# Kernel tuning notes

Hardware: AMD Instinct MI355X
Metric: run time of the kernel (lower is better)

## Reference

```python
import jax, jax.numpy as jnp
import numpy as np
import math

N_HEADS = 32
N_KV_HEADS = 4
HEAD_DIM = 128
N_REP = N_HEADS // N_KV_HEADS
ROPE_THETA = 10000.0
YARN_SCALE = 80.0
YARN_ALPHA = 1.0
YARN_BETA = 32.0
MAX_SEQ = int(2048 * YARN_SCALE)  # max_seq_len * yarn_scale, as in __init__


def _rope_yarn_cos_sin(S, dim):
    """Numpy (static) version of precompute_rope_yarn, sliced to S positions."""
    inv_freq = 1.0 / ROPE_THETA ** (np.arange(0, dim, 2, dtype=np.float32) / dim)
    wavelengths = 2.0 * math.pi / inv_freq
    r = MAX_SEQ / wavelengths
    gamma = np.clip((r - YARN_ALPHA) / (YARN_BETA - YARN_ALPHA), 0.0, 1.0)
    inv_freq = inv_freq * ((1.0 - gamma) / YARN_SCALE + gamma)
    t = np.arange(S, dtype=np.float32)
    freqs = np.outer(t, inv_freq)                      # [S, dim/2]
    emb = np.concatenate([freqs, freqs], axis=-1)      # [S, dim]
    emb = emb / math.sqrt(0.1 * math.log(YARN_SCALE) + 1.0)
    # broadcast shape [1, S, 1, dim] to apply per-position across heads
    return (jnp.asarray(np.cos(emb))[None, :, None, :],
            jnp.asarray(np.sin(emb))[None, :, None, :])


def _rotate_half(x):
    x1, x2 = jnp.split(x, 2, axis=-1)
    return jnp.concatenate([-x2, x1], axis=-1)


def setup_inputs() -> dict:
    key = jax.random.key(0)
    ks = jax.random.split(key, 5)
    B, S, D = 1, 2048, 4096
    sd = 1.0 / math.sqrt(D)
    return {
        "x": jax.random.normal(ks[0], (B, S, D), dtype=jnp.float32),
        "wq": jax.random.normal(ks[1], (D, N_HEADS * HEAD_DIM), dtype=jnp.float32) * sd,
        "wk": jax.random.normal(ks[2], (D, N_KV_HEADS * HEAD_DIM), dtype=jnp.float32) * sd,
        "wv": jax.random.normal(ks[3], (D, N_KV_HEADS * HEAD_DIM), dtype=jnp.float32) * sd,
        "wo": jax.random.normal(ks[4], (N_HEADS * HEAD_DIM, D), dtype=jnp.float32) * sd,
    }


def reference(x, wq, wk, wv, wo):
    B, S, D = x.shape
    scale = HEAD_DIM ** -0.5
    q = (x @ wq).reshape(B, S, N_HEADS, HEAD_DIM)
    k = (x @ wk).reshape(B, S, N_KV_HEADS, HEAD_DIM)
    v = (x @ wv).reshape(B, S, N_KV_HEADS, HEAD_DIM)
    cos, sin = _rope_yarn_cos_sin(S, HEAD_DIM)         # [1,S,1,Dh]
    q = q * cos + _rotate_half(q) * sin
    k = k * cos + _rotate_half(k) * sin
    # GQA: repeat kv heads to match query heads (repeat_interleave on head dim)
    k = jnp.repeat(k, N_REP, axis=2)
    v = jnp.repeat(v, N_REP, axis=2)
    # [B,H,S,Dh]
    q = q.transpose(0, 2, 1, 3)
    k = k.transpose(0, 2, 1, 3)
    v = v.transpose(0, 2, 1, 3)
    scores = jnp.einsum("bhsd,bhtd->bhst", q, k) * scale
    causal = jnp.tril(jnp.ones((S, S), dtype=bool))
    scores = jnp.where(causal[None, None], scores, jnp.finfo(scores.dtype).min)
    probs = jax.nn.softmax(scores, axis=-1)
    out = jnp.einsum("bhst,bhtd->bhsd", probs, v)
    out = out.transpose(0, 2, 1, 3).reshape(B, S, N_HEADS * HEAD_DIM)
    return out @ wo
```

## Files before the change

kernel.cpp:

```cpp
#include <hip/hip_runtime.h>
#include <math.h>

#define S_LEN 2048
#define D_MODEL 4096
#define NH 32
#define NKV 4
#define HD 128
#define KV_W (NKV * HD)
#define QK_W (D_MODEL + KV_W)
#define QKV_W (QK_W + KV_W)

typedef float f32x4 __attribute__((ext_vector_type(4)));
typedef __bf16 bf16x8 __attribute__((ext_vector_type(8)));

__device__ __forceinline__ void async16(const __bf16* g, __bf16* l) {
    __builtin_amdgcn_global_load_lds(
        (const __attribute__((address_space(1))) unsigned int*)g,
        (__attribute__((address_space(3))) unsigned int*)l, 16, 0, 0);
}

__global__ void cast_f32_bf16(const float* __restrict__ in, __bf16* __restrict__ out, int n) {
    int i = (blockIdx.x * blockDim.x + threadIdx.x) * 4;
    if (i >= n) return;
    float4 v = *reinterpret_cast<const float4*>(in + i);
    out[i + 0] = (__bf16)v.x;
    out[i + 1] = (__bf16)v.y;
    out[i + 2] = (__bf16)v.z;
    out[i + 3] = (__bf16)v.w;
}

__global__ void transpose_cast(const float* __restrict__ in, __bf16* __restrict__ out, int R, int C) {
    __shared__ float tile[32][33];
    int bx = blockIdx.x * 32, by = blockIdx.y * 32;
    int tx = threadIdx.x, ty = threadIdx.y;
#pragma unroll
    for (int i = 0; i < 32; i += 8)
        tile[ty + i][tx] = in[(size_t)(by + ty + i) * C + bx + tx];
    __syncthreads();
#pragma unroll
    for (int i = 0; i < 32; i += 8)
        out[(size_t)(bx + ty + i) * R + by + tx] = (__bf16)tile[tx][ty + i];
}

template <int MODE>
__global__ __launch_bounds__(256, 2) void gemm_bf16(const __bf16* __restrict__ A,
                                                    const __bf16* __restrict__ Bt,
                                                    void* __restrict__ Cp, void* __restrict__ Cp2,
                                                    int M, int N, int K) {
    __shared__ __bf16 a_lds[128 * 32];
    __shared__ __bf16 b_lds[128 * 32];

    const int tid = threadIdx.x;
    const int wave = tid >> 6, lane = tid & 63;
    const int quad = lane >> 4, l16 = lane & 15;
    const int wm = wave & 1, wn = wave >> 1;
    const int m0 = blockIdx.y * 128, n0 = blockIdx.x * 128;

    f32x4 acc[4][4];
#pragma unroll
    for (int i = 0; i < 4; i++)
#pragma unroll
        for (int j = 0; j < 4; j++) acc[i][j] = (f32x4)0.0f;

    const int crow = tid >> 2, ccol = (tid & 3) * 8;
    const __bf16* Ap0 = A + (size_t)(m0 + crow) * K + ccol;
    const __bf16* Ap1 = A + (size_t)(m0 + 64 + crow) * K + ccol;
    const __bf16* Bp0 = Bt + (size_t)(n0 + crow) * K + ccol;
    const __bf16* Bp1 = Bt + (size_t)(n0 + 64 + crow) * K + ccol;

    for (int k0 = 0; k0 < K; k0 += 32) {
        __syncthreads();
        async16(Ap0 + k0, a_lds + tid * 8);
        async16(Ap1 + k0, a_lds + (tid + 256) * 8);
        async16(Bp0 + k0, b_lds + tid * 8);
        async16(Bp1 + k0, b_lds + (tid + 256) * 8);
        __syncthreads();

        bf16x8 afr[4], bfr[4];
#pragma unroll
        for (int i = 0; i < 4; i++)
            afr[i] = *(const bf16x8*)(a_lds + (wm * 64 + i * 16 + l16) * 32 + quad * 8);
#pragma unroll
        for (int j = 0; j < 4; j++)
            bfr[j] = *(const bf16x8*)(b_lds + (wn * 64 + j * 16 + l16) * 32 + quad * 8);
#pragma unroll
        for (int i = 0; i < 4; i++)
#pragma unroll
            for (int j = 0; j < 4; j++)
                acc[i][j] = __builtin_amdgcn_mfma_f32_16x16x32_bf16(afr[i], bfr[j], acc[i][j], 0, 0, 0);
    }

    const bool vregion = (MODE == 1) && (n0 >= QK_W);
#pragma unroll
    for (int i = 0; i < 4; i++)
#pragma unroll
        for (int j = 0; j < 4; j++)
#pragma unroll
            for (int r = 0; r < 4; r++) {
                int gm = m0 + wm * 64 + i * 16 + quad * 4 + r;
                int gn = n0 + wn * 64 + j * 16 + l16;
                float v = acc[i][j][r];
                if constexpr (MODE == 0) {
                    ((float*)Cp)[(size_t)gm * N + gn] = v;
                } else {
                    if (vregion)
                        ((__bf16*)Cp2)[(size_t)(gn - QK_W) * M + gm] = (__bf16)v;
                    else
                        ((__bf16*)Cp)[(size_t)gm * QK_W + gn] = (__bf16)v;
                }
            }
}

__global__ void rope_cast(const __bf16* __restrict__ src, int sPitch, int sOff,
                          __bf16* __restrict__ dst, int dPitch, int H, int total) {
    int idx = blockIdx.x * blockDim.x + threadIdx.x;
    if (idx >= total) return;
    int d = idx & 63;
    int t = idx >> 6;
    int h = t % H;
    int s = t / H;

    float inv = __powf(10000.0f, -(float)d * (1.0f / 64.0f));
    float wl = 6.2831853071795864f / inv;
    float r = 163840.0f / wl;
    float gamma = fminf(fmaxf((r - 1.0f) * (1.0f / 31.0f), 0.0f), 1.0f);
    float adj = inv * ((1.0f - gamma) * (1.0f / 80.0f) + gamma);
    float ang = ((float)s * adj) / 1.1992508365439246f;
    float c = cosf(ang), sn = sinf(ang);

    const __bf16* b = src + (size_t)s * sPitch + sOff + h * HD;
    __bf16* o = dst + (size_t)s * dPitch + h * HD;
    float x1 = (float)b[d], x2 = (float)b[d + 64];
    o[d] = (__bf16)(x1 * c - x2 * sn);
    o[d + 64] = (__bf16)(x2 * c + x1 * sn);
}

__global__ __launch_bounds__(256, 2) void flash_attn(const __bf16* __restrict__ Q,
                                                     const __bf16* __restrict__ Kb,
                                                     const __bf16* __restrict__ Vt,
                                                     __bf16* __restrict__ O) {
    __shared__ __bf16 k_lds[64 * 128];
    __shared__ __bf16 vt_lds[128 * 64];
    __shared__ __bf16 p_lds[128 * 72];

    const int tid = threadIdx.x;
    const int wave = tid >> 6, lane = tid & 63;
    const int quad = lane >> 4, l16 = lane & 15;
    const int h = blockIdx.x;
    const int ty = blockIdx.y;
    const int t = (ty < 8) ? ty : 23 - ty;
    const int qb0 = t * 128;
    const int wrow = wave * 32;
    const int kvh = h >> 3;
    const float sl2e = 0.12752039149672056f;

    bf16x8 qfr[2][4];
#pragma unroll
    for (int mi = 0; mi < 2; mi++)
#pragma unroll
        for (int kk = 0; kk < 4; kk++)
            qfr[mi][kk] = *(const bf16x8*)(Q + (size_t)(qb0 + wrow + mi * 16 + l16) * D_MODEL
                                           + h * HD + kk * 32 + quad * 8);

    f32x4 acc[2][8];
#pragma unroll
    for (int mi = 0; mi < 2; mi++)
#pragma unroll
        for (int dt = 0; dt < 8; dt++) acc[mi][dt] = (f32x4)0.0f;
    float rs[2][4] = {{0.f, 0.f, 0.f, 0.f}, {0.f, 0.f, 0.f, 0.f}};

    const int nk = 2 * t + 2;
    for (int kt = 0; kt < nk; kt++) {
        const int k0 = kt * 64;
        __syncthreads();
#pragma unroll
        for (int it = 0; it < 4; it++) {
            int c = tid + it * 256;
            int krow = c >> 4, kcb = c & 15;
            async16(Kb + (size_t)(k0 + krow) * KV_W + kvh * HD + ((kcb ^ (krow & 15)) << 3),
                    k_lds + c * 8);
            int vrow = c >> 3, vcb = c & 7;
            async16(Vt + (size_t)(kvh * HD + vrow) * S_LEN + k0 + ((vcb ^ (vrow & 7)) << 3),
                    vt_lds + c * 8);
        }
        __syncthreads();

        f32x4 sc[2][4];
#pragma unroll
        for (int mi = 0; mi < 2; mi++)
#pragma unroll
            for (int j = 0; j < 4; j++) sc[mi][j] = (f32x4)0.0f;
#pragma unroll
        for (int j = 0; j < 4; j++)
#pragma unroll
            for (int kk = 0; kk < 4; kk++) {
                bf16x8 kf = *(const bf16x8*)(k_lds + (((j * 16 + l16) << 4) + ((kk * 4 + quad) ^ l16)) * 8);
                sc[0][j] = __builtin_amdgcn_mfma_f32_16x16x32_bf16(qfr[0][kk], kf, sc[0][j], 0, 0, 0);
                sc[1][j] = __builtin_amdgcn_mfma_f32_16x16x32_bf16(qfr[1][kk], kf, sc[1][j], 0, 0, 0);
            }

        const bool hasmask = (kt >= 2 * t);
#pragma unroll
        for (int mi = 0; mi < 2; mi++) {
            int rowb = qb0 + wrow + mi * 16 + quad * 4;
#pragma unroll
            for (int j = 0; j < 4; j++) {
                int kg = k0 + j * 16 + l16;
#pragma unroll
                for (int r = 0; r < 4; r++) {
                    float p = __builtin_amdgcn_exp2f(sc[mi][j][r] * sl2e);
                    if (hasmask && kg > rowb + r) p = 0.0f;
                    rs[mi][r] += p;
                    p_lds[(wrow + mi * 16 + quad * 4 + r) * 72 + j * 16 + l16] = (__bf16)p;
                }
            }
        }

        bf16x8 pf[2][2];
#pragma unroll
        for (int mi = 0; mi < 2; mi++)
#pragma unroll
            for (int kk = 0; kk < 2; kk++)
                pf[mi][kk] = *(const bf16x8*)(p_lds + (wrow + mi * 16 + l16) * 72 + kk * 32 + quad * 8);
#pragma unroll
        for (int dt = 0; dt < 8; dt++)
#pragma unroll
            for (int kk = 0; kk < 2; kk++) {
                bf16x8 vf = *(const bf16x8*)(vt_lds + (((dt * 16 + l16) << 3) + ((kk * 4 + quad) ^ (l16 & 7))) * 8);
                acc[0][dt] = __builtin_amdgcn_mfma_f32_16x16x32_bf16(pf[0][kk], vf, acc[0][dt], 0, 0, 0);
                acc[1][dt] = __builtin_amdgcn_mfma_f32_16x16x32_bf16(pf[1][kk], vf, acc[1][dt], 0, 0, 0);
            }
    }

    float inv_l[2][4];
#pragma unroll
    for (int mi = 0; mi < 2; mi++)
#pragma unroll
        for (int r = 0; r < 4; r++) {
            float s = rs[mi][r];
#pragma unroll
            for (int m = 1; m <= 8; m <<= 1) s += __shfl_xor(s, m, 64);
            inv_l[mi][r] = 1.0f / s;
        }

#pragma unroll
    for (int mi = 0; mi < 2; mi++)
#pragma unroll
        for (int dt = 0; dt < 8; dt++)
#pragma unroll
            for (int r = 0; r < 4; r++) {
                int row = qb0 + wrow + mi * 16 + quad * 4 + r;
                int col = h * HD + dt * 16 + l16;
                O[(size_t)row * D_MODEL + col] = (__bf16)(acc[mi][dt][r] * inv_l[mi][r]);
            }
}

extern "C" void kernel_launch(void* const* d_in, const int* in_sizes, int n_in,
                              void* d_out, int out_size, void* d_ws, size_t ws_size,
                              hipStream_t stream) {
    const float* x = (const float*)d_in[0];
    const float* wq = (const float*)d_in[1];
    const float* wk = (const float*)d_in[2];
    const float* wv = (const float*)d_in[3];
    const float* wo = (const float*)d_in[4];
    float* out = (float*)d_out;

    char* ws = (char*)d_ws;
    size_t off = 0;
    auto alloc = [&](size_t bytes) {
        void* p = ws + off;
        off += (bytes + 255) & ~(size_t)255;
        return p;
    };
    __bf16* xb    = (__bf16*)alloc((size_t)S_LEN * D_MODEL * 2);
    __bf16* wqkvT = (__bf16*)alloc((size_t)QKV_W * D_MODEL * 2);
    __bf16* woT   = (__bf16*)alloc((size_t)D_MODEL * D_MODEL * 2);
    __bf16* qkb   = (__bf16*)alloc((size_t)S_LEN * QK_W * 2);
    __bf16* vtb   = (__bf16*)alloc((size_t)KV_W * S_LEN * 2);
    __bf16* qb    = (__bf16*)alloc((size_t)S_LEN * D_MODEL * 2);
    __bf16* kb    = (__bf16*)alloc((size_t)S_LEN * KV_W * 2);
    __bf16* ob    = (__bf16*)alloc((size_t)S_LEN * D_MODEL * 2);

    cast_f32_bf16<<<(S_LEN * D_MODEL) / (256 * 4), 256, 0, stream>>>(x, xb, S_LEN * D_MODEL);
    transpose_cast<<<dim3(D_MODEL / 32, D_MODEL / 32), dim3(32, 8), 0, stream>>>(wq, wqkvT, D_MODEL, D_MODEL);
    transpose_cast<<<dim3(KV_W / 32, D_MODEL / 32), dim3(32, 8), 0, stream>>>(wk, wqkvT + (size_t)D_MODEL * D_MODEL, D_MODEL, KV_W);
    transpose_cast<<<dim3(KV_W / 32, D_MODEL / 32), dim3(32, 8), 0, stream>>>(wv, wqkvT + (size_t)QK_W * D_MODEL, D_MODEL, KV_W);
    transpose_cast<<<dim3(D_MODEL / 32, D_MODEL / 32), dim3(32, 8), 0, stream>>>(wo, woT, D_MODEL, D_MODEL);

    gemm_bf16<1><<<dim3(QKV_W / 128, S_LEN / 128), 256, 0, stream>>>(xb, wqkvT, qkb, vtb, S_LEN, QKV_W, D_MODEL);

    rope_cast<<<(S_LEN * NH * 64) / 256, 256, 0, stream>>>(qkb, QK_W, 0, qb, D_MODEL, NH, S_LEN * NH * 64);
    rope_cast<<<(S_LEN * NKV * 64) / 256, 256, 0, stream>>>(qkb, QK_W, D_MODEL, kb, KV_W, NKV, S_LEN * NKV * 64);

    flash_attn<<<dim3(NH, 16), 256, 0, stream>>>(qb, kb, vtb, ob);

    gemm_bf16<0><<<dim3(D_MODEL / 128, S_LEN / 128), 256, 0, stream>>>(ob, woT, out, nullptr, S_LEN, D_MODEL, D_MODEL);
}
```

Baseline: 499.2 us.

## Double-buffer GEMM and attention K tiles, vectorize weight transpose

The GEMM now keeps two LDS stages and issues the next K-slice's async loads before computing on the current one, which removes one barrier per iteration. Flash attention double-buffers the K tile: the V load overlaps the QK^T compute and the next K load overlaps the PV compute. The weight transpose kernel moves to 64x64 tiles with float4 loads and bf16x8 stores. The cost is more LDS per block, which could limit occupancy, plus extra barriers in the attention loop.

```diff
diff --git a/kernel.cpp b/kernel.cpp
--- a/kernel.cpp
+++ b/kernel.cpp
@@ -30,16 +30,27 @@
 }
 
 __global__ void transpose_cast(const float* __restrict__ in, __bf16* __restrict__ out, int R, int C) {
-    __shared__ float tile[32][33];
-    int bx = blockIdx.x * 32, by = blockIdx.y * 32;
-    int tx = threadIdx.x, ty = threadIdx.y;
-#pragma unroll
-    for (int i = 0; i < 32; i += 8)
-        tile[ty + i][tx] = in[(size_t)(by + ty + i) * C + bx + tx];
+    __shared__ float tile[64][65];
+    const int tid = threadIdx.x;
+    const int bx = blockIdx.x * 64, by = blockIdx.y * 64;
+#pragma unroll
+    for (int i = 0; i < 4; i++) {
+        int idx = tid + i * 256;
+        int r = idx >> 4, c4 = (idx & 15) * 4;
+        float4 v = *(const float4*)(in + (size_t)(by + r) * C + bx + c4);
+        tile[r][c4 + 0] = v.x; tile[r][c4 + 1] = v.y;
+        tile[r][c4 + 2] = v.z; tile[r][c4 + 3] = v.w;
+    }
     __syncthreads();
 #pragma unroll
-    for (int i = 0; i < 32; i += 8)
-        out[(size_t)(bx + ty + i) * R + by + tx] = (__bf16)tile[tx][ty + i];
+    for (int i = 0; i < 2; i++) {
+        int idx = tid + i * 256;
+        int oc = idx >> 3, r8 = (idx & 7) * 8;
+        bf16x8 v;
+#pragma unroll
+        for (int e = 0; e < 8; e++) v[e] = (__bf16)tile[r8 + e][oc];
+        *(bf16x8*)(out + (size_t)(bx + oc) * R + by + r8) = v;
+    }
 }
 
 template <int MODE>
@@ -47,8 +58,8 @@
                                                     const __bf16* __restrict__ Bt,
                                                     void* __restrict__ Cp, void* __restrict__ Cp2,
                                                     int M, int N, int K) {
-    __shared__ __bf16 a_lds[128 * 32];
-    __shared__ __bf16 b_lds[128 * 32];
+    __shared__ __bf16 a_lds[2][128 * 32];
+    __shared__ __bf16 b_lds[2][128 * 32];
 
     const int tid = threadIdx.x;
     const int wave = tid >> 6, lane = tid & 63;
@@ -68,21 +79,28 @@
     const __bf16* Bp0 = Bt + (size_t)(n0 + crow) * K + ccol;
     const __bf16* Bp1 = Bt + (size_t)(n0 + 64 + crow) * K + ccol;
 
+    async16(Ap0, a_lds[0] + tid * 8);
+    async16(Ap1, a_lds[0] + (tid + 256) * 8);
+    async16(Bp0, b_lds[0] + tid * 8);
+    async16(Bp1, b_lds[0] + (tid + 256) * 8);
+
     for (int k0 = 0; k0 < K; k0 += 32) {
+        const int cur = (k0 >> 5) & 1;
         __syncthreads();
-        async16(Ap0 + k0, a_lds + tid * 8);
-        async16(Ap1 + k0, a_lds + (tid + 256) * 8);
-        async16(Bp0 + k0, b_lds + tid * 8);
-        async16(Bp1 + k0, b_lds + (tid + 256) * 8);
-        __syncthreads();
+        if (k0 + 32 < K) {
+            async16(Ap0 + k0 + 32, a_lds[cur ^ 1] + tid * 8);
+            async16(Ap1 + k0 + 32, a_lds[cur ^ 1] + (tid + 256) * 8);
+            async16(Bp0 + k0 + 32, b_lds[cur ^ 1] + tid * 8);
+            async16(Bp1 + k0 + 32, b_lds[cur ^ 1] + (tid + 256) * 8);
+        }
 
         bf16x8 afr[4], bfr[4];
 #pragma unroll
         for (int i = 0; i < 4; i++)
-            afr[i] = *(const bf16x8*)(a_lds + (wm * 64 + i * 16 + l16) * 32 + quad * 8);
+            afr[i] = *(const bf16x8*)(a_lds[cur] + (wm * 64 + i * 16 + l16) * 32 + quad * 8);
 #pragma unroll
         for (int j = 0; j < 4; j++)
-            bfr[j] = *(const bf16x8*)(b_lds + (wn * 64 + j * 16 + l16) * 32 + quad * 8);
+            bfr[j] = *(const bf16x8*)(b_lds[cur] + (wn * 64 + j * 16 + l16) * 32 + quad * 8);
 #pragma unroll
         for (int i = 0; i < 4; i++)
 #pragma unroll
@@ -139,7 +157,7 @@
                                                      const __bf16* __restrict__ Kb,
                                                      const __bf16* __restrict__ Vt,
                                                      __bf16* __restrict__ O) {
-    __shared__ __bf16 k_lds[64 * 128];
+    __shared__ __bf16 k_lds[2][64 * 128];
     __shared__ __bf16 vt_lds[128 * 64];
     __shared__ __bf16 p_lds[128 * 72];
 
@@ -170,20 +188,27 @@
     float rs[2][4] = {{0.f, 0.f, 0.f, 0.f}, {0.f, 0.f, 0.f, 0.f}};
 
     const int nk = 2 * t + 2;
+
+#pragma unroll
+    for (int it = 0; it < 4; it++) {
+        int c = tid + it * 256;
+        int krow = c >> 4, kcb = c & 15;
+        async16(Kb + (size_t)krow * KV_W + kvh * HD + ((kcb ^ (krow & 15)) << 3),
+                k_lds[0] + c * 8);
+    }
+    __syncthreads();
+
     for (int kt = 0; kt < nk; kt++) {
         const int k0 = kt * 64;
-        __syncthreads();
+        const int cur = kt & 1;
+
 #pragma unroll
         for (int it = 0; it < 4; it++) {
             int c = tid + it * 256;
-            int krow = c >> 4, kcb = c & 15;
-            async16(Kb + (size_t)(k0 + krow) * KV_W + kvh * HD + ((kcb ^ (krow & 15)) << 3),
-                    k_lds + c * 8);
             int vrow = c >> 3, vcb = c & 7;
             async16(Vt + (size_t)(kvh * HD + vrow) * S_LEN + k0 + ((vcb ^ (vrow & 7)) << 3),
                     vt_lds + c * 8);
         }
-        __syncthreads();
 
         f32x4 sc[2][4];
 #pragma unroll
@@ -194,7 +219,7 @@
         for (int j = 0; j < 4; j++)
 #pragma unroll
             for (int kk = 0; kk < 4; kk++) {
-                bf16x8 kf = *(const bf16x8*)(k_lds + (((j * 16 + l16) << 4) + ((kk * 4 + quad) ^ l16)) * 8);
+                bf16x8 kf = *(const bf16x8*)(k_lds[cur] + (((j * 16 + l16) << 4) + ((kk * 4 + quad) ^ l16)) * 8);
                 sc[0][j] = __builtin_amdgcn_mfma_f32_16x16x32_bf16(qfr[0][kk], kf, sc[0][j], 0, 0, 0);
                 sc[1][j] = __builtin_amdgcn_mfma_f32_16x16x32_bf16(qfr[1][kk], kf, sc[1][j], 0, 0, 0);
             }
@@ -216,6 +241,18 @@
             }
         }
 
+        __syncthreads();
+
+        if (kt + 1 < nk) {
+#pragma unroll
+            for (int it = 0; it < 4; it++) {
+                int c = tid + it * 256;
+                int krow = c >> 4, kcb = c & 15;
+                async16(Kb + (size_t)(k0 + 64 + krow) * KV_W + kvh * HD + ((kcb ^ (krow & 15)) << 3),
+                        k_lds[cur ^ 1] + c * 8);
+            }
+        }
+
         bf16x8 pf[2][2];
 #pragma unroll
         for (int mi = 0; mi < 2; mi++)
@@ -230,6 +267,8 @@
                 acc[0][dt] = __builtin_amdgcn_mfma_f32_16x16x32_bf16(pf[0][kk], vf, acc[0][dt], 0, 0, 0);
                 acc[1][dt] = __builtin_amdgcn_mfma_f32_16x16x32_bf16(pf[1][kk], vf, acc[1][dt], 0, 0, 0);
             }
+
+        __syncthreads();
     }
 
     float inv_l[2][4];
@@ -282,10 +321,10 @@
     __bf16* ob    = (__bf16*)alloc((size_t)S_LEN * D_MODEL * 2);
 
     cast_f32_bf16<<<(S_LEN * D_MODEL) / (256 * 4), 256, 0, stream>>>(x, xb, S_LEN * D_MODEL);
-    transpose_cast<<<dim3(D_MODEL / 32, D_MODEL / 32), dim3(32, 8), 0, stream>>>(wq, wqkvT, D_MODEL, D_MODEL);
-    transpose_cast<<<dim3(KV_W / 32, D_MODEL / 32), dim3(32, 8), 0, stream>>>(wk, wqkvT + (size_t)D_MODEL * D_MODEL, D_MODEL, KV_W);
-    transpose_cast<<<dim3(KV_W / 32, D_MODEL / 32), dim3(32, 8), 0, stream>>>(wv, wqkvT + (size_t)QK_W * D_MODEL, D_MODEL, KV_W);
-    transpose_cast<<<dim3(D_MODEL / 32, D_MODEL / 32), dim3(32, 8), 0, stream>>>(wo, woT, D_MODEL, D_MODEL);
+    transpose_cast<<<dim3(D_MODEL / 64, D_MODEL / 64), 256, 0, stream>>>(wq, wqkvT, D_MODEL, D_MODEL);
+    transpose_cast<<<dim3(KV_W / 64, D_MODEL / 64), 256, 0, stream>>>(wk, wqkvT + (size_t)D_MODEL * D_MODEL, D_MODEL, KV_W);
+    transpose_cast<<<dim3(KV_W / 64, D_MODEL / 64), 256, 0, stream>>>(wv, wqkvT + (size_t)QK_W * D_MODEL, D_MODEL, KV_W);
+    transpose_cast<<<dim3(D_MODEL / 64, D_MODEL / 64), 256, 0, stream>>>(wo, woT, D_MODEL, D_MODEL);
 
     gemm_bf16<1><<<dim3(QKV_W / 128, S_LEN / 128), 256, 0, stream>>>(xb, wqkvT, qkb, vtb, S_LEN, QKV_W, D_MODEL);
 
```

Measured after the change: 496.6 us. Within noise of the previous version (-0.5%).
